# Kernel optimization log

Hardware: AMD Instinct MI355X
Metric: run time of the kernel (lower is better)

## Reference

```python
import jax, jax.numpy as jnp
import numpy as np

N_NODES = 50000
N_EDGES = 800000
N_GRAPHS = 512
VOCAB = 128
HID = 64
NCLS = 5


def _seg_mean(vals, ids, num_segments):
    s = jax.ops.segment_sum(vals, ids, num_segments=num_segments)
    cnt = jax.ops.segment_sum(jnp.ones((vals.shape[0],), vals.dtype), ids, num_segments=num_segments)
    return s / jnp.maximum(cnt, 1.0)[:, None]


def sage_conv(x, src, dst, W_l, b_l, W_r):
    # PyG SAGEConv (mean aggr): out = lin_l(mean_{j in N(i)} x_j) + lin_r(x_i)
    agg = _seg_mean(x[src], dst, x.shape[0])          # [N, H] gather + scatter-mean
    return agg @ W_l.T + b_l + x @ W_r.T


def setup_inputs() -> dict:
    key = jax.random.key(0)
    ks = jax.random.split(key, 10)
    scale = 1.0 / np.sqrt(HID)
    x_tokens = jax.random.randint(ks[0], (N_NODES,), 0, VOCAB)
    edge_index = jax.random.randint(ks[1], (2, N_EDGES), 0, N_NODES)
    batch = jnp.sort(jax.random.randint(ks[2], (N_NODES,), 0, N_GRAPHS))
    return {
        "x_tokens": x_tokens,
        "edge_index": edge_index,
        "batch": batch,
        "embed": jax.random.normal(ks[3], (VOCAB, HID), jnp.float32),
        "W1l": jax.random.normal(ks[4], (HID, HID), jnp.float32) * scale,
        "b1l": jnp.zeros((HID,), jnp.float32),
        "W1r": jax.random.normal(ks[5], (HID, HID), jnp.float32) * scale,
        "W2l": jax.random.normal(ks[6], (HID, HID), jnp.float32) * scale,
        "b2l": jnp.zeros((HID,), jnp.float32),
        "W2r": jax.random.normal(ks[7], (HID, HID), jnp.float32) * scale,
        "Wlin": jax.random.normal(ks[8], (NCLS, HID), jnp.float32) * scale,
        "blin": jnp.zeros((NCLS,), jnp.float32),
    }


def reference(x_tokens, edge_index, batch, embed, W1l, b1l, W1r, W2l, b2l, W2r, Wlin, blin):
    src, dst = edge_index[0], edge_index[1]
    x = embed[x_tokens]                                  # [N, H] embedding lookup
    x = jax.nn.relu(sage_conv(x, src, dst, W1l, b1l, W1r))
    x = jax.nn.relu(sage_conv(x, src, dst, W2l, b2l, W2r))
    g = _seg_mean(x, batch, N_GRAPHS)                    # global_mean_pool -> [G, H]
    return g @ Wlin.T + blin                             # [G, num_classes]
```

## Files before the change

kernel.cpp:

```cpp
#include <hip/hip_runtime.h>

#define N_NODES  50000
#define N_EDGES  800000
#define N_GRAPHS 512
#define HID      64
#define NCLS     5
#define NB       64
#define EST      36
#define AST      68

typedef __attribute__((ext_vector_type(8))) short bf16x8;
typedef __attribute__((ext_vector_type(4))) float f32x4;

__device__ inline unsigned short f2bf(float f) {
    unsigned int u = __builtin_bit_cast(unsigned int, f);
    unsigned int r = (u + 0x7FFFu + ((u >> 16) & 1u)) >> 16;
    return (unsigned short)r;
}
__device__ inline unsigned int packbf(float a, float b) {
    return (unsigned int)f2bf(a) | ((unsigned int)f2bf(b) << 16);
}
__device__ inline float bf2f(unsigned int u16) {
    unsigned int t = u16 << 16;
    return __builtin_bit_cast(float, t);
}

#define XCDS   8
#define NPX    (N_NODES / XCDS)
#define EPB    512
#define ECH2   ((N_EDGES + EPB - 1) / EPB)
#define SEC_E  (ECH2 * XCDS * 256)
#define E_T    (2 * 128 * 32)
#define PW_T   (64 * 64)
#define PREP_T (SEC_E + E_T + N_NODES + PW_T)
__global__ void k_prep_fill(
    const int* __restrict__ src, const int* __restrict__ dst,
    const int* __restrict__ tok,
    int* __restrict__ cnt, unsigned int* __restrict__ bucket,
    const float* __restrict__ embed,
    const float* __restrict__ W1l, const float* __restrict__ W1r,
    unsigned int* __restrict__ e1g,
    const int* __restrict__ batch,
    int* __restrict__ pos_start, int* __restrict__ pos_end,
    const float* __restrict__ W2l, const float* __restrict__ W2r,
    unsigned int* __restrict__ wb2) {
    int gid = blockIdx.x * blockDim.x + threadIdx.x;
    if (gid < SEC_E) {
        int blk   = gid >> 8;
        int tidl  = gid & 255;
        int range = blk & 7;
        int chunk = blk >> 3;
        int lo = range * NPX;
        int e0 = chunk * EPB + tidl;
        int e1 = e0 + 256;
        int d0 = (e0 < N_EDGES) ? dst[e0] : -1;
        int d1 = (e1 < N_EDGES) ? dst[e1] : -1;
        int s0 = (e0 < N_EDGES) ? src[e0] : 0;
        int s1 = (e1 < N_EDGES) ? src[e1] : 0;
        bool k0 = (d0 >= lo) && (d0 < lo + NPX);
        bool k1 = (d1 >= lo) && (d1 < lo + NPX);
        unsigned int t0 = k0 ? (unsigned int)tok[s0] : 0u;
        unsigned int t1 = k1 ? (unsigned int)tok[s1] : 0u;
        if (k0) {
            int pos = atomicAdd(&cnt[d0], 1);
            if (pos < NB) bucket[(long)d0 * NB + pos] = (unsigned int)s0 | (t0 << 16);
        }
        if (k1) {
            int pos = atomicAdd(&cnt[d1], 1);
            if (pos < NB) bucket[(long)d1 * NB + pos] = (unsigned int)s1 | (t1 << 16);
        }
        return;
    }
    gid -= SEC_E;
    if (gid < E_T) {
        int idx = gid & 4095;
        int t = idx >> 5, c = idx & 31;
        const float* W = (gid < 4096) ? W1l : W1r;
        const float* e  = embed + (long)t * HID;
        const float* w0 = W + (long)(2 * c) * HID;
        const float* w1 = w0 + HID;
        float a0 = 0.f, a1 = 0.f;
#pragma unroll 8
        for (int k = 0; k < HID; ++k) {
            float ev = e[k];
            a0 += ev * w0[k];
            a1 += ev * w1[k];
        }
        e1g[gid] = packbf(a0, a1);
        return;
    }
    gid -= E_T;
    if (gid < N_NODES) {
        int n = gid;
        int b = batch[n];
        if (n == 0 || batch[n - 1] != b) pos_start[b] = n;
        if (n == N_NODES - 1 || batch[n + 1] != b) pos_end[b] = n + 1;
        return;
    }
    gid -= N_NODES;
    if (gid < PW_T) {
        int h = gid >> 6, c = gid & 63;
        float2 v = (c < 32) ? ((const float2*)(W2l + (long)h * HID))[c]
                            : ((const float2*)(W2r + (long)h * HID))[c - 32];
        wb2[gid] = packbf(v.x, v.y);
    }
}

#define NPB1 64
__global__ __launch_bounds__(512) void k_layer1(
    const int* __restrict__ cnt, const unsigned int* __restrict__ bucket,
    const int* __restrict__ tok, const unsigned int* __restrict__ e1g,
    const float* __restrict__ bl, unsigned int* __restrict__ x1b)
{
    __shared__ unsigned int el[128 * EST];
    const int tid  = threadIdx.x;
    const int wv   = tid >> 6;
    const int lane = tid & 63;
    const int n0   = blockIdx.x * NPB1;

    for (int i = tid; i < 4096; i += 512) {
        int t = i >> 5, c = i & 31;
        el[t * EST + c] = e1g[i];
    }
    __syncthreads();

    const int q  = lane & 7;
    const int e8 = lane >> 3;

    int degA[8]; unsigned int vA[8]; int tkA[8];
#pragma unroll
    for (int i = 0; i < 8; ++i) {
        int nn = n0 + wv * 8 + i;
        int nc = min(nn, N_NODES - 1);
        degA[i] = cnt[nc];
        vA[i]   = bucket[(long)nc * NB + lane];
        tkA[i]  = tok[nc];
    }

#pragma unroll
    for (int i = 0; i < 8; ++i) {
        int nn = n0 + wv * 8 + i;
        int m  = (nn < N_NODES) ? min(degA[i], NB) : 0;
        float f0 = 0, f1 = 0, f2 = 0, f3 = 0, f4 = 0, f5 = 0, f6 = 0, f7 = 0;
#pragma unroll
        for (int g = 0; g < 8; ++g) {
            int j = g * 8 + e8;
            unsigned int vv = __shfl(vA[i], j, 64);
            if (j < m) {
                uint4 w4 = *(const uint4*)(el + (vv >> 16) * EST + q * 4);
                f0 += bf2f(w4.x & 0xffff); f1 += bf2f(w4.x >> 16);
                f2 += bf2f(w4.y & 0xffff); f3 += bf2f(w4.y >> 16);
                f4 += bf2f(w4.z & 0xffff); f5 += bf2f(w4.z >> 16);
                f6 += bf2f(w4.w & 0xffff); f7 += bf2f(w4.w >> 16);
            }
        }
#pragma unroll
        for (int o = 8; o < 64; o <<= 1) {
            f0 += __shfl_xor(f0, o, 64); f1 += __shfl_xor(f1, o, 64);
            f2 += __shfl_xor(f2, o, 64); f3 += __shfl_xor(f3, o, 64);
            f4 += __shfl_xor(f4, o, 64); f5 += __shfl_xor(f5, o, 64);
            f6 += __shfl_xor(f6, o, 64); f7 += __shfl_xor(f7, o, 64);
        }
        if (e8 == 0 && nn < N_NODES) {
            float inv = 1.0f / (float)max(degA[i], 1);
            uint4 sv = *(const uint4*)(e1g + 4096 + tkA[i] * 32 + q * 4);
            float4 b0 = *(const float4*)(bl + q * 8);
            float4 b1 = *(const float4*)(bl + q * 8 + 4);
            uint4 o;
            o.x = packbf(fmaxf(f0 * inv + bf2f(sv.x & 0xffff) + b0.x, 0.f),
                         fmaxf(f1 * inv + bf2f(sv.x >> 16)    + b0.y, 0.f));
            o.y = packbf(fmaxf(f2 * inv + bf2f(sv.y & 0xffff) + b0.z, 0.f),
                         fmaxf(f3 * inv + bf2f(sv.y >> 16)    + b0.w, 0.f));
            o.z = packbf(fmaxf(f4 * inv + bf2f(sv.z & 0xffff) + b1.x, 0.f),
                         fmaxf(f5 * inv + bf2f(sv.z >> 16)    + b1.y, 0.f));
            o.w = packbf(fmaxf(f6 * inv + bf2f(sv.w & 0xffff) + b1.z, 0.f),
                         fmaxf(f7 * inv + bf2f(sv.w >> 16)    + b1.w, 0.f));
            *(uint4*)(x1b + (long)nn * 32 + q * 4) = o;
        }
    }
}

__global__ __launch_bounds__(256) void k_layer2(
    const int* __restrict__ cnt, const unsigned int* __restrict__ bucket,
    const unsigned int* __restrict__ xb,
    const unsigned int* __restrict__ wb, const float* __restrict__ bl,
    const int* __restrict__ batch, float* __restrict__ gacc)
{
    __shared__ unsigned int As[16 * AST];
    const int tid  = threadIdx.x;
    const int wv   = tid >> 6;
    const int lane = tid & 63;
    const int n0   = blockIdx.x * 16;

    const int q  = lane & 7;
    const int e8 = lane >> 3;

    int degA[4]; unsigned int vA[4]; int mA[4]; int ncA[4];
#pragma unroll
    for (int i = 0; i < 4; ++i) {
        int nn = n0 + wv * 4 + i;
        int nc = min(nn, N_NODES - 1);
        ncA[i] = nc;
        degA[i] = cnt[nc];
        vA[i] = bucket[(long)nc * NB + lane];
    }
#pragma unroll
    for (int i = 0; i < 4; ++i) {
        int nn = n0 + wv * 4 + i;
        mA[i] = (nn < N_NODES) ? min(degA[i], NB) : 0;
    }

#pragma unroll
    for (int i = 0; i < 4; ++i) {
        int rl = wv * 4 + i;
        int m  = mA[i];
        uint4 w4[8];
#pragma unroll
        for (int g = 0; g < 8; ++g) {
            int j = g * 8 + e8;
            unsigned int vv = __shfl(vA[i], j, 64);
            vv = (j < m) ? vv : 0u;
            w4[g] = *((const uint4*)(xb + (long)(vv & 0xffffu) * 32) + q);
        }
        float f0 = 0, f1 = 0, f2 = 0, f3 = 0, f4 = 0, f5 = 0, f6 = 0, f7 = 0;
#pragma unroll
        for (int g = 0; g < 8; ++g) {
            int j = g * 8 + e8;
            if (j < m) {
                f0 += bf2f(w4[g].x & 0xffff); f1 += bf2f(w4[g].x >> 16);
                f2 += bf2f(w4[g].y & 0xffff); f3 += bf2f(w4[g].y >> 16);
                f4 += bf2f(w4[g].z & 0xffff); f5 += bf2f(w4[g].z >> 16);
                f6 += bf2f(w4[g].w & 0xffff); f7 += bf2f(w4[g].w >> 16);
            }
        }
#pragma unroll
        for (int o = 8; o < 64; o <<= 1) {
            f0 += __shfl_xor(f0, o, 64); f1 += __shfl_xor(f1, o, 64);
            f2 += __shfl_xor(f2, o, 64); f3 += __shfl_xor(f3, o, 64);
            f4 += __shfl_xor(f4, o, 64); f5 += __shfl_xor(f5, o, 64);
            f6 += __shfl_xor(f6, o, 64); f7 += __shfl_xor(f7, o, 64);
        }
        if (e8 == 0) {
            float inv = 1.0f / (float)max(degA[i], 1);
            uint4 o;
            o.x = packbf(f0 * inv, f1 * inv);
            o.y = packbf(f2 * inv, f3 * inv);
            o.z = packbf(f4 * inv, f5 * inv);
            o.w = packbf(f6 * inv, f7 * inv);
            *(uint4*)(As + rl * AST + q * 4) = o;
        } else if (e8 == 1) {
            uint4 sv = *((const uint4*)(xb + (long)ncA[i] * 32) + q);
            *(uint4*)(As + rl * AST + 32 + q * 4) = sv;
        }
    }
    __syncthreads();

    const int t    = wv;
    const int mm   = lane & 15;
    const int quad = lane >> 4;

    bf16x8 afr[4];
#pragma unroll
    for (int kst = 0; kst < 4; ++kst)
        afr[kst] = *(const bf16x8*)(As + mm * AST + kst * 16 + quad * 4);

    f32x4 acc = (f32x4){0.f, 0.f, 0.f, 0.f};
#pragma unroll
    for (int kst = 0; kst < 4; ++kst) {
        bf16x8 bfr = *(const bf16x8*)(wb + (t * 16 + mm) * 64 + kst * 16 + quad * 4);
        acc = __builtin_amdgcn_mfma_f32_16x16x32_bf16(bfr, afr[kst], acc, 0, 0, 0);
    }

    int node = n0 + mm;
    int hb = t * 16 + quad * 4;
    float4 bb = *(const float4*)(bl + hb);
    float a0 = fmaxf(acc[0] + bb.x, 0.f);
    float a1 = fmaxf(acc[1] + bb.y, 0.f);
    float a2 = fmaxf(acc[2] + bb.z, 0.f);
    float a3 = fmaxf(acc[3] + bb.w, 0.f);

    int g = batch[node];
#pragma unroll
    for (int off = 1; off < 16; off <<= 1) {
        float o0 = __shfl_up(a0, off, 16), o1 = __shfl_up(a1, off, 16);
        float o2 = __shfl_up(a2, off, 16), o3 = __shfl_up(a3, off, 16);
        int   og = __shfl_up(g, off, 16);
        if (mm >= off && og == g) { a0 += o0; a1 += o1; a2 += o2; a3 += o3; }
    }
    int gn = __shfl_down(g, 1, 16);
    if (mm == 15 || gn != g) {
        float* dp = gacc + g * HID + hb;
        unsafeAtomicAdd(dp + 0, a0);
        unsafeAtomicAdd(dp + 1, a1);
        unsafeAtomicAdd(dp + 2, a2);
        unsafeAtomicAdd(dp + 3, a3);
    }
}

__global__ __launch_bounds__(256) void k_head(
    const float* __restrict__ gacc,
    const int* __restrict__ pstart, const int* __restrict__ pend,
    const float* __restrict__ Wlin, const float* __restrict__ blin,
    float* __restrict__ out)
{
    int g = blockIdx.x * blockDim.x + threadIdx.x;
    if (g >= N_GRAPHS) return;
    float inv = 1.0f / (float)max(pend[g] - pstart[g], 1);
    float s0 = 0, s1 = 0, s2 = 0, s3 = 0, s4 = 0;
    const float* row = gacc + g * HID;
#pragma unroll 8
    for (int k = 0; k < HID; ++k) {
        float mk = row[k] * inv;
        s0 += mk * Wlin[0 * HID + k];
        s1 += mk * Wlin[1 * HID + k];
        s2 += mk * Wlin[2 * HID + k];
        s3 += mk * Wlin[3 * HID + k];
        s4 += mk * Wlin[4 * HID + k];
    }
    out[g * NCLS + 0] = s0 + blin[0];
    out[g * NCLS + 1] = s1 + blin[1];
    out[g * NCLS + 2] = s2 + blin[2];
    out[g * NCLS + 3] = s3 + blin[3];
    out[g * NCLS + 4] = s4 + blin[4];
}

extern "C" void kernel_launch(void* const* d_in, const int* in_sizes, int n_in,
                              void* d_out, int out_size, void* d_ws, size_t ws_size,
                              hipStream_t stream) {
    const int*   tok   = (const int*)d_in[0];
    const int*   eidx  = (const int*)d_in[1];
    const int*   batch = (const int*)d_in[2];
    const float* embed = (const float*)d_in[3];
    const float* W1l   = (const float*)d_in[4];
    const float* b1l   = (const float*)d_in[5];
    const float* W1r   = (const float*)d_in[6];
    const float* W2l   = (const float*)d_in[7];
    const float* b2l   = (const float*)d_in[8];
    const float* W2r   = (const float*)d_in[9];
    const float* Wlin  = (const float*)d_in[10];
    const float* blin  = (const float*)d_in[11];
    float* out = (float*)d_out;

    const int* src = eidx;
    const int* dst = eidx + N_EDGES;

    char* wsp = (char*)d_ws;
    size_t off = 0;
    auto alloc = [&](size_t bytes) -> void* {
        void* p = wsp + off;
        off = (off + bytes + 255) & ~(size_t)255;
        return p;
    };
    int*   cnt     = (int*)  alloc((size_t)N_NODES * 4);
    int*   pstart  = (int*)  alloc((size_t)N_GRAPHS * 4);
    int*   pend    = (int*)  alloc((size_t)N_GRAPHS * 4);
    float* gacc    = (float*)alloc((size_t)N_GRAPHS * HID * 4);
    unsigned int* bucket = (unsigned int*)alloc((size_t)N_NODES * NB * 4);
    unsigned int* x1b    = (unsigned int*)alloc((size_t)N_NODES * 32 * 4);
    unsigned int* e1g    = (unsigned int*)alloc((size_t)E_T * 4);
    unsigned int* wb2    = (unsigned int*)alloc((size_t)PW_T * 4);

    hipMemsetAsync(cnt, 0, ((char*)gacc + (size_t)N_GRAPHS * HID * 4) - (char*)cnt, stream);

    k_prep_fill<<<(PREP_T + 255) / 256, 256, 0, stream>>>(
        src, dst, tok, cnt, bucket,
        embed, W1l, W1r, e1g, batch, pstart, pend, W2l, W2r, wb2);

    k_layer1<<<(N_NODES + NPB1 - 1) / NPB1, 512, 0, stream>>>(
        cnt, bucket, tok, e1g, b1l, x1b);
    k_layer2<<<N_NODES / 16, 256, 0, stream>>>(
        cnt, bucket, x1b, wb2, b2l, batch, gacc);

    k_head<<<(N_GRAPHS + 255) / 256, 256, 0, stream>>>(
        gacc, pstart, pend, Wlin, blin, out);
}
```

Before: 187.0 us.

## Fuse classifier head into layer-2 epilogue via linear projection atomics

```diff
diff --git a/kernel.cpp b/kernel.cpp
--- a/kernel.cpp
+++ b/kernel.cpp
@@ -32,7 +32,8 @@
 #define SEC_E  (ECH2 * XCDS * 256)
 #define E_T    (2 * 128 * 32)
 #define PW_T   (64 * 64)
-#define PREP_T (SEC_E + E_T + N_NODES + PW_T)
+#define OUT_T  (N_GRAPHS * NCLS)
+#define PREP_T (SEC_E + E_T + N_NODES + PW_T + OUT_T)
 __global__ void k_prep_fill(
     const int* __restrict__ src, const int* __restrict__ dst,
     const int* __restrict__ tok,
@@ -43,7 +44,8 @@
     const int* __restrict__ batch,
     int* __restrict__ pos_start, int* __restrict__ pos_end,
     const float* __restrict__ W2l, const float* __restrict__ W2r,
-    unsigned int* __restrict__ wb2) {
+    unsigned int* __restrict__ wb2,
+    const float* __restrict__ blin, float* __restrict__ out) {
     int gid = blockIdx.x * blockDim.x + threadIdx.x;
     if (gid < SEC_E) {
         int blk   = gid >> 8;
@@ -103,6 +105,11 @@
         float2 v = (c < 32) ? ((const float2*)(W2l + (long)h * HID))[c]
                             : ((const float2*)(W2r + (long)h * HID))[c - 32];
         wb2[gid] = packbf(v.x, v.y);
+        return;
+    }
+    gid -= PW_T;
+    if (gid < OUT_T) {
+        out[gid] = blin[gid % NCLS];
     }
 }
 
@@ -184,7 +191,9 @@
     const int* __restrict__ cnt, const unsigned int* __restrict__ bucket,
     const unsigned int* __restrict__ xb,
     const unsigned int* __restrict__ wb, const float* __restrict__ bl,
-    const int* __restrict__ batch, float* __restrict__ gacc)
+    const int* __restrict__ batch,
+    const int* __restrict__ pstart, const int* __restrict__ pend,
+    const float* __restrict__ Wlin, float* __restrict__ out)
 {
     __shared__ unsigned int As[16 * AST];
     const int tid  = threadIdx.x;
@@ -289,39 +298,14 @@
     }
     int gn = __shfl_down(g, 1, 16);
     if (mm == 15 || gn != g) {
-        float* dp = gacc + g * HID + hb;
-        unsafeAtomicAdd(dp + 0, a0);
-        unsafeAtomicAdd(dp + 1, a1);
-        unsafeAtomicAdd(dp + 2, a2);
-        unsafeAtomicAdd(dp + 3, a3);
-    }
-}
-
-__global__ __launch_bounds__(256) void k_head(
-    const float* __restrict__ gacc,
-    const int* __restrict__ pstart, const int* __restrict__ pend,
-    const float* __restrict__ Wlin, const float* __restrict__ blin,
-    float* __restrict__ out)
-{
-    int g = blockIdx.x * blockDim.x + threadIdx.x;
-    if (g >= N_GRAPHS) return;
-    float inv = 1.0f / (float)max(pend[g] - pstart[g], 1);
-    float s0 = 0, s1 = 0, s2 = 0, s3 = 0, s4 = 0;
-    const float* row = gacc + g * HID;
-#pragma unroll 8
-    for (int k = 0; k < HID; ++k) {
-        float mk = row[k] * inv;
-        s0 += mk * Wlin[0 * HID + k];
-        s1 += mk * Wlin[1 * HID + k];
-        s2 += mk * Wlin[2 * HID + k];
-        s3 += mk * Wlin[3 * HID + k];
-        s4 += mk * Wlin[4 * HID + k];
-    }
-    out[g * NCLS + 0] = s0 + blin[0];
-    out[g * NCLS + 1] = s1 + blin[1];
-    out[g * NCLS + 2] = s2 + blin[2];
-    out[g * NCLS + 3] = s3 + blin[3];
-    out[g * NCLS + 4] = s4 + blin[4];
+        float invg = 1.0f / (float)max(pend[g] - pstart[g], 1);
+#pragma unroll
+        for (int c = 0; c < NCLS; ++c) {
+            const float* wr = Wlin + c * HID + hb;
+            float p = (a0 * wr[0] + a1 * wr[1] + a2 * wr[2] + a3 * wr[3]) * invg;
+            unsafeAtomicAdd(out + g * NCLS + c, p);
+        }
+    }
 }
 
 extern "C" void kernel_launch(void* const* d_in, const int* in_sizes, int n_in,
@@ -354,23 +338,19 @@
     int*   cnt     = (int*)  alloc((size_t)N_NODES * 4);
     int*   pstart  = (int*)  alloc((size_t)N_GRAPHS * 4);
     int*   pend    = (int*)  alloc((size_t)N_GRAPHS * 4);
-    float* gacc    = (float*)alloc((size_t)N_GRAPHS * HID * 4);
     unsigned int* bucket = (unsigned int*)alloc((size_t)N_NODES * NB * 4);
     unsigned int* x1b    = (unsigned int*)alloc((size_t)N_NODES * 32 * 4);
     unsigned int* e1g    = (unsigned int*)alloc((size_t)E_T * 4);
     unsigned int* wb2    = (unsigned int*)alloc((size_t)PW_T * 4);
 
-    hipMemsetAsync(cnt, 0, ((char*)gacc + (size_t)N_GRAPHS * HID * 4) - (char*)cnt, stream);
+    hipMemsetAsync(cnt, 0, (size_t)N_NODES * 4, stream);
 
     k_prep_fill<<<(PREP_T + 255) / 256, 256, 0, stream>>>(
         src, dst, tok, cnt, bucket,
-        embed, W1l, W1r, e1g, batch, pstart, pend, W2l, W2r, wb2);
+        embed, W1l, W1r, e1g, batch, pstart, pend, W2l, W2r, wb2, blin, out);
 
     k_layer1<<<(N_NODES + NPB1 - 1) / NPB1, 512, 0, stream>>>(
         cnt, bucket, tok, e1g, b1l, x1b);
     k_layer2<<<N_NODES / 16, 256, 0, stream>>>(
-        cnt, bucket, x1b, wb2, b2l, batch, gacc);
-
-    k_head<<<(N_GRAPHS + 255) / 256, 256, 0, stream>>>(
-        gacc, pstart, pend, Wlin, blin, out);
-}
+        cnt, bucket, x1b, wb2, b2l, batch, pstart, pend, Wlin, out);
+}
```

New measurement: 283.3 us. +51.5%, slower.
